# Kernel tuning notes

Hardware: AMD Instinct MI355X
Metric: run time of the kernel (lower is better)

Reference implementation:

```python
import jax, jax.numpy as jnp
import numpy as np

B, S, H = 2, 2048, 1024
NH, NKV, HD = 16, 4, 64

def setup_inputs() -> dict:
    key = jax.random.key(0)
    k1, k2, k3, k4, k5 = jax.random.split(key, 5)
    return {
        "hidden_states": jax.random.normal(k1, (B, S, H), dtype=jnp.float32),
        "attention_mask": jnp.ones((B, S), dtype=jnp.int32),
        "wq": jax.random.normal(k2, (H, NH * HD), dtype=jnp.float32) * 0.02,
        "wk": jax.random.normal(k3, (H, NKV * HD), dtype=jnp.float32) * 0.02,
        "wv": jax.random.normal(k4, (H, NKV * HD), dtype=jnp.float32) * 0.02,
        "wo": jax.random.normal(k5, (NH * HD, 1), dtype=jnp.float32) * 0.02,
    }

def reference(hidden_states, attention_mask, wq, wk, wv, wo):
    bsz, seq_len, _ = hidden_states.shape
    n_rep = NH // NKV
    # projections -> (b, h, s, d)
    q = (hidden_states @ wq).reshape(bsz, seq_len, NH, HD).transpose(0, 2, 1, 3)
    k = (hidden_states @ wk).reshape(bsz, seq_len, NKV, HD).transpose(0, 2, 1, 3)
    v = (hidden_states @ wv).reshape(bsz, seq_len, NKV, HD).transpose(0, 2, 1, 3)
    # repeat_kv == repeat_interleave along head axis
    k = jnp.repeat(k, n_rep, axis=1)
    v = jnp.repeat(v, n_rep, axis=1)
    scores = jnp.einsum('bhqd,bhkd->bhqk', q, k) / np.sqrt(HD).astype(np.float32)
    mask = attention_mask[:, None, None, :]  # (b,1,1,k)
    scores = jnp.where(mask == 0, jnp.float32(-jnp.inf), scores)
    attn = jax.nn.softmax(scores, axis=-1)
    out = jnp.einsum('bhqk,bhkd->bqhd', attn, v).reshape(bsz, seq_len, NH * HD)
    return out @ wo  # (b, s, 1)
```

## Files before the change

### kernel.cpp

```cpp
#include <hip/hip_runtime.h>
#include <stdint.h>


typedef __bf16 bf16x8 __attribute__((ext_vector_type(8)));
typedef float f32x4 __attribute__((ext_vector_type(4)));
typedef float f32x2 __attribute__((ext_vector_type(2)));

__device__ inline unsigned short f2bf(float f) {
    unsigned int u = __builtin_bit_cast(unsigned int, f);
    u += 0x7fff + ((u >> 16) & 1);
    return (unsigned short)(u >> 16);
}
__device__ inline bf16x8 ldfrag(const unsigned short* p) {
    uint4 v = *(const uint4*)p;
    return __builtin_bit_cast(bf16x8, v);
}
__device__ inline void gl2lds16(const void* g, void* l) {
    __builtin_amdgcn_global_load_lds(
        (const __attribute__((address_space(1))) void*)g,
        (__attribute__((address_space(3))) void*)l, 16, 0, 0);
}

#define SCALE_Q 0.18033688011112042f

__global__ __launch_bounds__(256) void prep_kernel(
    const float* __restrict__ wq, const float* __restrict__ wk,
    const float* __restrict__ wv, const float* __restrict__ wo,
    unsigned short* __restrict__ wT)
{
    int bid = blockIdx.x, tid = threadIdx.x;
    if (bid < 320) {
        __shared__ float tile[64 * 65];
        int t = bid;
        int ntile = t / 16, ctile = t % 16;
        int nb = ntile * 64, cb = ctile * 64;
        int tx = tid & 63, ty = tid >> 6;
        for (int i = 0; i < 16; i++) {
            int cl = i * 4 + ty;
            int n = nb + tx;
            float v = (n < 1024) ? wq[(cb + cl) * 1024 + n] * SCALE_Q
                                 : wk[(cb + cl) * 256 + (n - 1024)];
            tile[cl * 65 + tx] = v;
        }
        __syncthreads();
        for (int i = 0; i < 16; i++) {
            int nl = i * 4 + ty;
            wT[(nb + nl) * 1024 + cb + tx] = f2bf(tile[tx * 65 + nl]);
        }
    } else {
        int u = (bid - 320) * 256 + tid;
        int n2 = u >> 10, c = u & 1023;
        if (n2 < 16) {
            int h = n2, kv = h >> 2;
            const float* wvr = wv + c * 256 + kv * 64;
            const float* wor = wo + h * 64;
            float s = 0.f;
            #pragma unroll 8
            for (int d = 0; d < 64; d++) s += wvr[d] * wor[d];
            wT[(1280 + n2) * 1024 + c] = f2bf(s);
        } else {
            wT[(1280 + n2) * 1024 + c] = 0;
        }
    }
}

__global__ __launch_bounds__(256) void gemm_kernel(
    const float* __restrict__ hs, const unsigned short* __restrict__ wT,
    unsigned short* __restrict__ Qp, unsigned short* __restrict__ Kp,
    float* __restrict__ vproj)
{
    __shared__ __align__(16) unsigned short Al[3][128 * 32];
    __shared__ __align__(16) unsigned short Bl[3][64 * 32];
    int p = blockIdx.x + 11 * blockIdx.y;
    int xcd = p & 7;
    int j = p >> 3;
    int rt = (xcd << 3) + j / 11;
    int nt = j % 11;
    int tid = threadIdx.x;
    int lane = tid & 63, w = tid >> 6;
    int l15 = lane & 15, quad = lane >> 4;
    int wm = (w >> 1) * 64, wn = (w & 1) * 32;

    f32x4 acc[4][2];
    const f32x4 zero = {0.f, 0.f, 0.f, 0.f};
    for (int i = 0; i < 4; i++) for (int j2 = 0; j2 < 2; j2++) acc[i][j2] = zero;

    int arow = nt * 128, rrow = rt * 64;
    int srowA = w * 32 + (lane >> 2);
    int scolA = (lane & 3) * 8;
    const unsigned short* ga = wT + (size_t)(arow + srowA) * 1024 + scolA;
    int lofsA = (w * 32) * 32;
    int rWl = w * 16 + (lane >> 2);
    const float* gb = hs + (size_t)(rrow + rWl) * 1024 + (lane & 3) * 8;
    int bwofs = rWl * 32 + (lane & 3) * 8;

    float4 r0a, r0b, r1a, r1b, r2a, r2b;

#define STAGE_A(SB) \
    gl2lds16(ga,             Al[SB] + lofsA); \
    gl2lds16(ga + 16 * 1024, Al[SB] + lofsA + 16 * 32); \
    ga += 32;

#define LOAD_B(RA, RB) \
    RA = *(const float4*)gb; RB = *(const float4*)(gb + 4); gb += 32;

#define CVT_WRITE_B(SB, RA, RB) { \
    bf16x8 t; \
    t[0] = (__bf16)RA.x; t[1] = (__bf16)RA.y; t[2] = (__bf16)RA.z; t[3] = (__bf16)RA.w; \
    t[4] = (__bf16)RB.x; t[5] = (__bf16)RB.y; t[6] = (__bf16)RB.z; t[7] = (__bf16)RB.w; \
    *(bf16x8*)(Bl[SB] + bwofs) = t; }

#define GEMM_COMPUTE(CB) { \
    bf16x8 af[4], bfr[2]; \
    for (int i = 0; i < 4; i++) \
        af[i] = ldfrag(Al[CB] + (wm + i * 16 + l15) * 32 + quad * 8); \
    for (int j2 = 0; j2 < 2; j2++) \
        bfr[j2] = ldfrag(Bl[CB] + (wn + j2 * 16 + l15) * 32 + quad * 8); \
    for (int i = 0; i < 4; i++) \
        for (int j2 = 0; j2 < 2; j2++) \
            acc[i][j2] = __builtin_amdgcn_mfma_f32_16x16x32_bf16(af[i], bfr[j2], acc[i][j2], 0, 0, 0); }

#define GITER(C, S2, W, RS2A, RS2B, RWA, RWB) \
    STAGE_A(S2) \
    LOAD_B(RS2A, RS2B) \
    asm volatile("s_waitcnt vmcnt(4)" ::: "memory"); \
    CVT_WRITE_B(W, RWA, RWB) \
    asm volatile("s_waitcnt lgkmcnt(0)" ::: "memory"); \
    __builtin_amdgcn_s_barrier(); \
    GEMM_COMPUTE(C) \
    __builtin_amdgcn_s_barrier();

    STAGE_A(0) LOAD_B(r0a, r0b)
    STAGE_A(1) LOAD_B(r1a, r1b)
    asm volatile("s_waitcnt vmcnt(4)" ::: "memory");
    CVT_WRITE_B(0, r0a, r0b)

    for (int kt = 0; kt < 10; kt++) {
        GITER(0, 2, 1, r2a, r2b, r1a, r1b)
        GITER(1, 0, 2, r0a, r0b, r2a, r2b)
        GITER(2, 1, 0, r1a, r1b, r0a, r0b)
    }
    asm volatile("s_waitcnt vmcnt(0)" ::: "memory");
    CVT_WRITE_B(1, r1a, r1b)
    asm volatile("s_waitcnt lgkmcnt(0)" ::: "memory");
    __builtin_amdgcn_s_barrier();
    GEMM_COMPUTE(0)
    GEMM_COMPUTE(1)

#undef STAGE_A
#undef LOAD_B
#undef CVT_WRITE_B
#undef GEMM_COMPUTE
#undef GITER

    for (int i = 0; i < 4; i++) {
        for (int j2 = 0; j2 < 2; j2++) {
            int nw = nt * 128 + wm + i * 16 + quad * 4;
            int r  = rt * 64 + wn + j2 * 16 + l15;
            if (nt < 8) {
                ushort4 o;
                o.x = f2bf(acc[i][j2][0]); o.y = f2bf(acc[i][j2][1]);
                o.z = f2bf(acc[i][j2][2]); o.w = f2bf(acc[i][j2][3]);
                *(ushort4*)(Qp + (size_t)r * 1024 + nw) = o;
            } else if (nt < 10) {
                ushort4 o;
                o.x = f2bf(acc[i][j2][0]); o.y = f2bf(acc[i][j2][1]);
                o.z = f2bf(acc[i][j2][2]); o.w = f2bf(acc[i][j2][3]);
                *(ushort4*)(Kp + (size_t)r * 256 + (nw - 1024)) = o;
            } else {
                for (int rg = 0; rg < 4; rg++) {
                    int h = nw + rg - 1280;
                    if (h < 16)
                        vproj[((size_t)(r >> 11) * 16 + h) * 2048 + (r & 2047)] = acc[i][j2][rg];
                }
            }
        }
    }
}

__global__ __launch_bounds__(256) void attn_kernel(
    const unsigned short* __restrict__ Qp, const unsigned short* __restrict__ Kp,
    const float* __restrict__ vproj, const int* __restrict__ mask,
    float2* __restrict__ part)
{
    __shared__ __align__(16) unsigned short Kl[256 * 64];
    __shared__ __align__(16) float vpml[4 * 256];
    __shared__ __align__(16) float biasl[256];
    int qt = blockIdx.x;
    int b = blockIdx.y >> 2, kv = blockIdx.y & 3;
    int ks = blockIdx.z;
    int tid = threadIdx.x, lane = tid & 63, w = tid >> 6;
    int l15 = lane & 15, quad = lane >> 4;
    int h = kv * 4 + w;
    int k0 = ks * 256;
    int qrow0 = qt * 64;

    {
        int swz = (lane & 7) ^ ((lane >> 3) & 7);
        const unsigned short* kbase =
            Kp + (size_t)(b * 2048 + k0 + w * 64 + (lane >> 3)) * 256 + kv * 64 + swz * 8;
        unsigned short* ldst = Kl + (w * 64) * 64;
        #pragma unroll
        for (int j = 0; j < 8; j++)
            gl2lds16(kbase + (size_t)(j * 8) * 256, ldst + j * 8 * 64);
    }

    bf16x8 qf[4][2];
    for (int qs = 0; qs < 4; qs++) {
        const unsigned short* qp =
            Qp + (size_t)(b * 2048 + qrow0 + qs * 16 + l15) * 1024 + h * 64 + quad * 8;
        qf[qs][0] = ldfrag(qp);
        qf[qs][1] = ldfrag(qp + 32);
    }

    {
        int h2 = tid >> 6, kk = (tid & 63) * 4;
        *(float4*)(vpml + h2 * 256 + kk) =
            *(const float4*)(vproj + ((size_t)b * 16 + kv * 4 + h2) * 2048 + k0 + kk);
    }
    if (tid < 64) {
        int4 mm = *(const int4*)(mask + b * 2048 + k0 + tid * 4);
        float4 bb;
        bb.x = mm.x ? 0.f : -30000.f;
        bb.y = mm.y ? 0.f : -30000.f;
        bb.z = mm.z ? 0.f : -30000.f;
        bb.w = mm.w ? 0.f : -30000.f;
        *(float4*)(biasl + tid * 4) = bb;
    }
    __syncthreads();

    f32x2 nd[4];
    const f32x2 zero2 = {0.f, 0.f};
    for (int qs = 0; qs < 4; qs++) nd[qs] = zero2;

    for (int t8 = 0; t8 < 16; t8++) {
        int r0 = t8 * 16 + l15;
        int rx = r0 & 7;
        bf16x8 a0 = ldfrag(Kl + r0 * 64 + ((quad ^ rx) * 8));
        bf16x8 a1 = ldfrag(Kl + r0 * 64 + (((quad ^ rx) ^ 4) * 8));
        f32x4 vpm4 = *(const f32x4*)(vpml + w * 256 + t8 * 16 + quad * 4);
        f32x4 c4   = *(const f32x4*)(biasl + t8 * 16 + quad * 4);
        for (int qs = 0; qs < 4; qs++) {
            __builtin_amdgcn_s_setprio(1);
            f32x4 d = __builtin_amdgcn_mfma_f32_16x16x32_bf16(a0, qf[qs][0], c4, 0, 0, 0);
            d = __builtin_amdgcn_mfma_f32_16x16x32_bf16(a1, qf[qs][1], d, 0, 0, 0);
            __builtin_amdgcn_s_setprio(0);
            for (int r = 0; r < 4; r++) {
                float e = __builtin_amdgcn_exp2f(d[r]);
                f32x2 m = {vpm4[r], 1.0f};
                nd[qs] += m * e;
            }
        }
    }
    for (int qs = 0; qs < 4; qs++) {
        float n = nd[qs][0], dd = nd[qs][1];
        n += __shfl_xor(n, 16);  n += __shfl_xor(n, 32);
        dd += __shfl_xor(dd, 16); dd += __shfl_xor(dd, 32);
        if (quad == 0) {
            int q = qrow0 + qs * 16 + l15;
            part[((size_t)(b * 2048 + q) * 16 + h) * 8 + ks] = make_float2(n, dd);
        }
    }
}

__global__ __launch_bounds__(256) void combine_kernel(
    const float2* __restrict__ part, float* __restrict__ out)
{
    int wid = (blockIdx.x * 256 + threadIdx.x) >> 6;
    int lane = threadIdx.x & 63;
    const float2* base = part + (size_t)wid * 128;
    float2 p0 = base[lane];
    float2 p1 = base[64 + lane];
    for (int m = 1; m <= 4; m <<= 1) {
        p0.x += __shfl_xor(p0.x, m); p0.y += __shfl_xor(p0.y, m);
        p1.x += __shfl_xor(p1.x, m); p1.y += __shfl_xor(p1.y, m);
    }
    float v = p0.x / p0.y + p1.x / p1.y;
    for (int m = 8; m <= 32; m <<= 1) v += __shfl_xor(v, m);
    if (lane == 0) out[wid] = v;
}

extern "C" void kernel_launch(void* const* d_in, const int* in_sizes, int n_in,
                              void* d_out, int out_size, void* d_ws, size_t ws_size,
                              hipStream_t stream)
{
    const float* hs  = (const float*)d_in[0];
    const int* mask  = (const int*)d_in[1];
    const float* wq  = (const float*)d_in[2];
    const float* wk  = (const float*)d_in[3];
    const float* wv  = (const float*)d_in[4];
    const float* wo  = (const float*)d_in[5];

    char* ws = (char*)d_ws;
    unsigned short* wT = (unsigned short*)ws;
    unsigned short* Qp = (unsigned short*)(ws + 2883584);
    unsigned short* Kp = (unsigned short*)(ws + 11272192);
    float* vproj       = (float*)(ws + 13369344);
    float2* part       = (float2*)(ws + 13631488);

    prep_kernel<<<832, 256, 0, stream>>>(wq, wk, wv, wo, wT);
    gemm_kernel<<<dim3(11, 64), 256, 0, stream>>>(hs, wT, Qp, Kp, vproj);
    attn_kernel<<<dim3(32, 8, 8), 256, 0, stream>>>(Qp, Kp, vproj, mask, part);
    combine_kernel<<<1024, 256, 0, stream>>>(part, (float*)d_out);
}
```

Before: 136.2 us.

## Fuse combine into attention via last-block counter and deepen GEMM LDS ring

```diff
diff --git a/kernel.cpp b/kernel.cpp
--- a/kernel.cpp
+++ b/kernel.cpp
@@ -26,7 +26,7 @@
 __global__ __launch_bounds__(256) void prep_kernel(
     const float* __restrict__ wq, const float* __restrict__ wk,
     const float* __restrict__ wv, const float* __restrict__ wo,
-    unsigned short* __restrict__ wT)
+    unsigned short* __restrict__ wT, int* __restrict__ cnt)
 {
     int bid = blockIdx.x, tid = threadIdx.x;
     if (bid < 320) {
@@ -48,6 +48,8 @@
             wT[(nb + nl) * 1024 + cb + tx] = f2bf(tile[tx * 65 + nl]);
         }
     } else {
+        if (bid == 320 && tid < 64)
+            __hip_atomic_store(cnt + tid, 0, __ATOMIC_RELAXED, __HIP_MEMORY_SCOPE_AGENT);
         int u = (bid - 320) * 256 + tid;
         int n2 = u >> 10, c = u & 1023;
         if (n2 < 16) {
@@ -69,8 +71,8 @@
     unsigned short* __restrict__ Qp, unsigned short* __restrict__ Kp,
     float* __restrict__ vproj)
 {
-    __shared__ __align__(16) unsigned short Al[3][128 * 32];
-    __shared__ __align__(16) unsigned short Bl[3][64 * 32];
+    __shared__ __align__(16) unsigned short Al[4][128 * 32];
+    __shared__ __align__(16) unsigned short Bl[4][64 * 32];
     int p = blockIdx.x + 11 * blockIdx.y;
     int xcd = p & 7;
     int j = p >> 3;
@@ -94,7 +96,7 @@
     const float* gb = hs + (size_t)(rrow + rWl) * 1024 + (lane & 3) * 8;
     int bwofs = rWl * 32 + (lane & 3) * 8;
 
-    float4 r0a, r0b, r1a, r1b, r2a, r2b;
+    float4 e0a, e0b, e1a, e1b;
 
 #define STAGE_A(SB) \
     gl2lds16(ga,             Al[SB] + lofsA); \
@@ -120,38 +122,40 @@
         for (int j2 = 0; j2 < 2; j2++) \
             acc[i][j2] = __builtin_amdgcn_mfma_f32_16x16x32_bf16(af[i], bfr[j2], acc[i][j2], 0, 0, 0); }
 
-#define GITER(C, S2, W, RS2A, RS2B, RWA, RWB) \
+#define GITER1(C, S2, W, LA, LB, WA, WB) \
     STAGE_A(S2) \
-    LOAD_B(RS2A, RS2B) \
+    LOAD_B(LA, LB) \
     asm volatile("s_waitcnt vmcnt(4)" ::: "memory"); \
-    CVT_WRITE_B(W, RWA, RWB) \
+    CVT_WRITE_B(W, WA, WB) \
     asm volatile("s_waitcnt lgkmcnt(0)" ::: "memory"); \
     __builtin_amdgcn_s_barrier(); \
-    GEMM_COMPUTE(C) \
-    __builtin_amdgcn_s_barrier();
-
-    STAGE_A(0) LOAD_B(r0a, r0b)
-    STAGE_A(1) LOAD_B(r1a, r1b)
+    GEMM_COMPUTE(C)
+
+    STAGE_A(0) LOAD_B(e0a, e0b)
+    STAGE_A(1) LOAD_B(e1a, e1b)
     asm volatile("s_waitcnt vmcnt(4)" ::: "memory");
-    CVT_WRITE_B(0, r0a, r0b)
-
-    for (int kt = 0; kt < 10; kt++) {
-        GITER(0, 2, 1, r2a, r2b, r1a, r1b)
-        GITER(1, 0, 2, r0a, r0b, r2a, r2b)
-        GITER(2, 1, 0, r1a, r1b, r0a, r0b)
-    }
+    CVT_WRITE_B(0, e0a, e0b)
+
+    for (int kt = 0; kt < 7; kt++) {
+        GITER1(0, 2, 1, e0a, e0b, e1a, e1b)
+        GITER1(1, 3, 2, e1a, e1b, e0a, e0b)
+        GITER1(2, 0, 3, e0a, e0b, e1a, e1b)
+        GITER1(3, 1, 0, e1a, e1b, e0a, e0b)
+    }
+    GITER1(0, 2, 1, e0a, e0b, e1a, e1b)
+    GITER1(1, 3, 2, e1a, e1b, e0a, e0b)
     asm volatile("s_waitcnt vmcnt(0)" ::: "memory");
-    CVT_WRITE_B(1, r1a, r1b)
+    CVT_WRITE_B(3, e1a, e1b)
     asm volatile("s_waitcnt lgkmcnt(0)" ::: "memory");
     __builtin_amdgcn_s_barrier();
-    GEMM_COMPUTE(0)
-    GEMM_COMPUTE(1)
+    GEMM_COMPUTE(2)
+    GEMM_COMPUTE(3)
 
 #undef STAGE_A
 #undef LOAD_B
 #undef CVT_WRITE_B
 #undef GEMM_COMPUTE
-#undef GITER
+#undef GITER1
 
     for (int i = 0; i < 4; i++) {
         for (int j2 = 0; j2 < 2; j2++) {
@@ -181,11 +185,12 @@
 __global__ __launch_bounds__(256) void attn_kernel(
     const unsigned short* __restrict__ Qp, const unsigned short* __restrict__ Kp,
     const float* __restrict__ vproj, const int* __restrict__ mask,
-    float2* __restrict__ part)
+    float2* __restrict__ part, int* __restrict__ cnt, float* __restrict__ out)
 {
     __shared__ __align__(16) unsigned short Kl[256 * 64];
     __shared__ __align__(16) float vpml[4 * 256];
     __shared__ __align__(16) float biasl[256];
+    __shared__ int lastflag;
     int qt = blockIdx.x;
     int b = blockIdx.y >> 2, kv = blockIdx.y & 3;
     int ks = blockIdx.z;
@@ -258,26 +263,40 @@
         dd += __shfl_xor(dd, 16); dd += __shfl_xor(dd, 32);
         if (quad == 0) {
             int q = qrow0 + qs * 16 + l15;
-            part[((size_t)(b * 2048 + q) * 16 + h) * 8 + ks] = make_float2(n, dd);
-        }
-    }
-}
-
-__global__ __launch_bounds__(256) void combine_kernel(
-    const float2* __restrict__ part, float* __restrict__ out)
-{
-    int wid = (blockIdx.x * 256 + threadIdx.x) >> 6;
-    int lane = threadIdx.x & 63;
-    const float2* base = part + (size_t)wid * 128;
-    float2 p0 = base[lane];
-    float2 p1 = base[64 + lane];
-    for (int m = 1; m <= 4; m <<= 1) {
-        p0.x += __shfl_xor(p0.x, m); p0.y += __shfl_xor(p0.y, m);
-        p1.x += __shfl_xor(p1.x, m); p1.y += __shfl_xor(p1.y, m);
-    }
-    float v = p0.x / p0.y + p1.x / p1.y;
-    for (int m = 8; m <= 32; m <<= 1) v += __shfl_xor(v, m);
-    if (lane == 0) out[wid] = v;
+            unsigned long long bits =
+                __builtin_bit_cast(unsigned long long, make_float2(n, dd));
+            __hip_atomic_store(
+                (unsigned long long*)(part + (((size_t)(b * 2048 + q) * 16 + h) * 8 + ks)),
+                bits, __ATOMIC_RELAXED, __HIP_MEMORY_SCOPE_AGENT);
+        }
+    }
+
+    asm volatile("s_waitcnt vmcnt(0)" ::: "memory");
+    __syncthreads();
+    if (tid == 0)
+        lastflag = (__hip_atomic_fetch_add(cnt + (b * 32 + qt), 1,
+                        __ATOMIC_RELAXED, __HIP_MEMORY_SCOPE_AGENT) == 31);
+    __syncthreads();
+    if (lastflag) {
+        for (int i = 0; i < 16; i++) {
+            int q = qrow0 + w * 16 + i;
+            const unsigned long long* pb =
+                (const unsigned long long*)(part + (size_t)(b * 2048 + q) * 128);
+            unsigned long long u0 = __hip_atomic_load(pb + lane,
+                __ATOMIC_RELAXED, __HIP_MEMORY_SCOPE_AGENT);
+            unsigned long long u1 = __hip_atomic_load(pb + 64 + lane,
+                __ATOMIC_RELAXED, __HIP_MEMORY_SCOPE_AGENT);
+            float2 p0 = __builtin_bit_cast(float2, u0);
+            float2 p1 = __builtin_bit_cast(float2, u1);
+            for (int m = 1; m <= 4; m <<= 1) {
+                p0.x += __shfl_xor(p0.x, m); p0.y += __shfl_xor(p0.y, m);
+                p1.x += __shfl_xor(p1.x, m); p1.y += __shfl_xor(p1.y, m);
+            }
+            float v = p0.x / p0.y + p1.x / p1.y;
+            for (int m = 8; m <= 32; m <<= 1) v += __shfl_xor(v, m);
+            if (lane == 0) out[b * 2048 + q] = v;
+        }
+    }
 }
 
 extern "C" void kernel_launch(void* const* d_in, const int* in_sizes, int n_in,
@@ -297,9 +316,9 @@
     unsigned short* Kp = (unsigned short*)(ws + 11272192);
     float* vproj       = (float*)(ws + 13369344);
     float2* part       = (float2*)(ws + 13631488);
-
-    prep_kernel<<<832, 256, 0, stream>>>(wq, wk, wv, wo, wT);
+    int* cnt           = (int*)(ws + 17825792);
+
+    prep_kernel<<<832, 256, 0, stream>>>(wq, wk, wv, wo, wT, cnt);
     gemm_kernel<<<dim3(11, 64), 256, 0, stream>>>(hs, wT, Qp, Kp, vproj);
-    attn_kernel<<<dim3(32, 8, 8), 256, 0, stream>>>(Qp, Kp, vproj, mask, part);
-    combine_kernel<<<1024, 256, 0, stream>>>(part, (float*)d_out);
-}
+    attn_kernel<<<dim3(32, 8, 8), 256, 0, stream>>>(Qp, Kp, vproj, mask, part, cnt, (float*)d_out);
+}
```

Result: slower. 144.3 us (+6.0%).
